# Performance work log

Hardware: AMD Instinct MI355X
Metric: run time of the kernel (lower is better)

Reference implementation:

```python
import jax, jax.numpy as jnp
import numpy as np

N_NODES = 50000
N_EDGES = 200000
N_GRAPHS = 2048
EMB = 300
N_LAYERS = 5
BN_EPS = 1e-5


def setup_inputs() -> dict:
    key = jax.random.key(0)
    ks = jax.random.split(key, 16)
    s = 0.02
    d = {}
    d["atomic_number"] = jax.random.randint(ks[0], (N_NODES,), 0, 120)
    d["chirality_type"] = jax.random.randint(ks[1], (N_NODES,), 0, 3)
    d["bond_type"] = jax.random.randint(ks[2], (N_EDGES,), 0, 6)
    d["bond_direction_type"] = jax.random.randint(ks[3], (N_EDGES,), 0, 3)
    d["src"] = jax.random.randint(ks[4], (N_EDGES,), 0, N_NODES)
    d["dst"] = jax.random.randint(ks[5], (N_EDGES,), 0, N_NODES)
    d["graph_ids"] = jnp.sort(jax.random.randint(ks[6], (N_NODES,), 0, N_GRAPHS))
    d["num_graphs"] = N_GRAPHS
    d["node_emb0"] = jax.random.normal(ks[7], (120, EMB), jnp.float32) * s
    d["node_emb1"] = jax.random.normal(ks[8], (3, EMB), jnp.float32) * s
    d["edge_emb0"] = jax.random.normal(ks[9], (N_LAYERS, 6, EMB), jnp.float32) * s
    d["edge_emb1"] = jax.random.normal(ks[10], (N_LAYERS, 3, EMB), jnp.float32) * s
    d["W1"] = jax.random.normal(ks[11], (N_LAYERS, EMB, 2 * EMB), jnp.float32) * s
    d["b1"] = jnp.zeros((N_LAYERS, 2 * EMB), jnp.float32)
    d["W2"] = jax.random.normal(ks[12], (N_LAYERS, 2 * EMB, EMB), jnp.float32) * s
    d["b2"] = jnp.zeros((N_LAYERS, EMB), jnp.float32)
    d["bn_gamma"] = jnp.ones((N_LAYERS, EMB), jnp.float32)
    d["bn_beta"] = jnp.zeros((N_LAYERS, EMB), jnp.float32)
    d["bn_mean"] = jax.random.normal(ks[13], (N_LAYERS, EMB), jnp.float32) * s
    d["bn_var"] = jax.random.uniform(ks[14], (N_LAYERS, EMB), jnp.float32, 0.5, 1.5)
    return d


def gin_node_feats(atomic_number, chirality_type, bond_type, bond_direction_type,
                   src, dst, node_emb0, node_emb1, edge_emb0, edge_emb1,
                   W1, b1, W2, b2, bn_gamma, bn_beta, bn_mean, bn_var):
    n = atomic_number.shape[0]
    h = node_emb0[atomic_number] + node_emb1[chirality_type]  # [N, EMB]
    feats = [h]
    for l in range(N_LAYERS):
        # u_add_e message: src node feat + per-layer categorical edge embedding
        e = edge_emb0[l][bond_type] + edge_emb1[l][bond_direction_type]  # [E, EMB]
        m = feats[l][src] + e
        agg = jax.ops.segment_sum(m, dst, num_segments=n)  # sum aggregation at dst
        x = jax.nn.relu(agg @ W1[l] + b1[l]) @ W2[l] + b2[l]  # GIN MLP 300->600->300
        # BatchNorm1d in eval mode (running stats)
        x = (x - bn_mean[l]) * jax.lax.rsqrt(bn_var[l] + BN_EPS) * bn_gamma[l] + bn_beta[l]
        if l < N_LAYERS - 1:
            x = jax.nn.relu(x)  # activation on all but last layer
        feats.append(x)  # dropout is identity in eval mode
    return jnp.concatenate(feats, axis=1)  # JK='concat' -> [N, 6*EMB]


def reference(atomic_number, chirality_type, bond_type, bond_direction_type,
              src, dst, graph_ids, num_graphs,
              node_emb0, node_emb1, edge_emb0, edge_emb1,
              W1, b1, W2, b2, bn_gamma, bn_beta, bn_mean, bn_var):
    nf = gin_node_feats(atomic_number, chirality_type, bond_type, bond_direction_type,
                        src, dst, node_emb0, node_emb1, edge_emb0, edge_emb1,
                        W1, b1, W2, b2, bn_gamma, bn_beta, bn_mean, bn_var)
    sums = jax.ops.segment_sum(nf, graph_ids, num_segments=num_graphs)  # SumPooling
    counts = jax.ops.segment_sum(jnp.ones((nf.shape[0], 1), nf.dtype), graph_ids,
                                 num_segments=num_graphs)
    avg = sums / jnp.maximum(counts, 1.0)  # AvgPooling
    return jnp.concatenate([avg, sums], axis=1)  # [G, 2*6*EMB]
```

## Files before the change

### kernel.cpp

```cpp
#include <hip/hip_runtime.h>

#define EMB 300
#define HID 600
#define NL 5
#define BN_EPS 1e-5f

#define FS 320
#define HS 640
#define NPW 8
#define KS1 10
#define KS2 20

typedef __attribute__((ext_vector_type(8))) short short8;
typedef __attribute__((ext_vector_type(4))) float f32x4;
typedef __attribute__((ext_vector_type(4))) unsigned short us4;

__device__ __forceinline__ unsigned short f2bf(float x) {
    unsigned u = __float_as_uint(x);
    unsigned r = (u + 0x7FFFu + ((u >> 16) & 1u)) >> 16;
    return (unsigned short)r;
}
__device__ __forceinline__ float bf2f(unsigned short h) {
    return __uint_as_float(((unsigned)h) << 16);
}

#define GLDS16(gsrc, ldst)                                                     \
    __builtin_amdgcn_global_load_lds(                                          \
        (const __attribute__((address_space(1))) unsigned int*)(gsrc),         \
        (__attribute__((address_space(3))) unsigned int*)(ldst), 16, 0, 0)

__global__ void k_init_h0(const int* __restrict__ an, const int* __restrict__ ch,
                          const float* __restrict__ ne0, const float* __restrict__ ne1,
                          unsigned short* __restrict__ Fb, int n) {
    int t = blockIdx.x * blockDim.x + threadIdx.x;
    int i = t / (FS / 4), f4 = t - i * (FS / 4);
    if (i >= n) return;
    int f = f4 * 4;
    us4 h = {0, 0, 0, 0};
    if (f < EMB) {
        const float4 a = *(const float4*)(ne0 + (size_t)an[i] * EMB + f);
        const float4 b = *(const float4*)(ne1 + (size_t)ch[i] * EMB + f);
        h[0] = f2bf(a.x + b.x); h[1] = f2bf(a.y + b.y);
        h[2] = f2bf(a.z + b.z); h[3] = f2bf(a.w + b.w);
    }
    *(us4*)(Fb + (size_t)i * FS + f) = h;
}

__global__ void k_hist(const int* __restrict__ dst, const int* __restrict__ bt,
                       const int* __restrict__ bd, int* __restrict__ deg,
                       int* __restrict__ cnt9, int e) {
    int t = blockIdx.x * blockDim.x + threadIdx.x;
    if (t >= e) return;
    int d = dst[t];
    atomicAdd(&deg[d], 1);
    atomicAdd(&cnt9[d * 9 + bt[t]], 1);
    atomicAdd(&cnt9[d * 9 + 6 + bd[t]], 1);
}

__global__ __launch_bounds__(256)
void k_scan_blk(const int* __restrict__ deg, int* __restrict__ incl,
                int* __restrict__ part, int n) {
    int tid = threadIdx.x;
    int base = blockIdx.x * 1024 + tid * 4;
    int v0 = (base + 0 < n) ? deg[base + 0] : 0;
    int v1 = (base + 1 < n) ? deg[base + 1] : 0;
    int v2 = (base + 2 < n) ? deg[base + 2] : 0;
    int v3 = (base + 3 < n) ? deg[base + 3] : 0;
    int ts = v0 + v1 + v2 + v3;
    int lane = tid & 63, w = tid >> 6;
    int x = ts;
#pragma unroll
    for (int off = 1; off < 64; off <<= 1) {
        int y = __shfl_up(x, off);
        if (lane >= off) x += y;
    }
    __shared__ int ws[4];
    if (lane == 63) ws[w] = x;
    __syncthreads();
    int woff = 0;
    for (int i = 0; i < w; ++i) woff += ws[i];
    int r = woff + x - ts;
    r += v0; if (base + 0 < n) incl[base + 0] = r;
    r += v1; if (base + 1 < n) incl[base + 1] = r;
    r += v2; if (base + 2 < n) incl[base + 2] = r;
    r += v3; if (base + 3 < n) incl[base + 3] = r;
    if (tid == 255) part[blockIdx.x] = woff + x;
}

__global__ __launch_bounds__(1024)
void k_scan_part(int* __restrict__ part, int nb) {
    int tid = threadIdx.x;
    int v = (tid < nb) ? part[tid] : 0;
    int lane = tid & 63, w = tid >> 6;
    int x = v;
#pragma unroll
    for (int off = 1; off < 64; off <<= 1) {
        int y = __shfl_up(x, off);
        if (lane >= off) x += y;
    }
    __shared__ int ws[16];
    if (lane == 63) ws[w] = x;
    __syncthreads();
    int woff = 0;
    for (int i = 0; i < w; ++i) woff += ws[i];
    if (tid < nb) part[tid] = woff + x - v;
}

__global__ void k_scan_add(const int* __restrict__ incl, const int* __restrict__ part,
                           const int* __restrict__ deg, int* __restrict__ roff,
                           int* __restrict__ curs, int n) {
    int i = blockIdx.x * blockDim.x + threadIdx.x;
    if (i >= n) return;
    int inc = incl[i] + part[i >> 10];
    roff[i + 1] = inc;
    curs[i] = inc - deg[i];
    if (i == 0) roff[0] = 0;
}

__global__ void k_scatter(const int* __restrict__ dst, const int* __restrict__ src,
                          int* __restrict__ cursor, int* __restrict__ srcs, int e) {
    int t = blockIdx.x * blockDim.x + threadIdx.x;
    if (t < e) { int p = atomicAdd(&cursor[dst[t]], 1); srcs[p] = src[t]; }
}

__global__ void k_gbound(const int* __restrict__ gids, int* __restrict__ gstart,
                         int n, int G) {
    int i = blockIdx.x * blockDim.x + threadIdx.x;
    if (i >= n) return;
    int g = gids[i];
    int gp = (i == 0) ? -1 : gids[i - 1];
    for (int q = gp + 1; q <= g; ++q) gstart[q] = i;
    if (i == n - 1)
        for (int q = g + 1; q <= G; ++q) gstart[q] = n;
}

__global__ void k_prep_w1p(const float* __restrict__ W1, unsigned short* __restrict__ W1P,
                           int total) {
    int t = blockIdx.x * blockDim.x + threadIdx.x;
    if (t >= total) return;
    int lane = t & 63;
    int r = t >> 6;
    int ks = r % KS1; r /= KS1;
    int nf = r % 40;
    int l = r / 40;
    int n = nf * 16 + (lane & 15);
    int kb = ks * 32 + (lane >> 4) * 8;
    unsigned short v[8];
#pragma unroll
    for (int e = 0; e < 8; ++e) {
        int k = kb + e;
        v[e] = (n < HID && k < EMB) ? f2bf(W1[(size_t)l * EMB * HID + (size_t)k * HID + n]) : 0;
    }
    *(short8*)(W1P + (size_t)t * 8) = *(short8*)v;
}

__global__ void k_prep_w2p(const float* __restrict__ W2, unsigned short* __restrict__ W2P,
                           int total) {
    int t = blockIdx.x * blockDim.x + threadIdx.x;
    if (t >= total) return;
    int lane = t & 63;
    int r = t >> 6;
    int ks = r % KS2; r /= KS2;
    int nf = r % 20;
    int l = r / 20;
    int n = nf * 16 + (lane & 15);
    int kb = ks * 32 + (lane >> 4) * 8;
    unsigned short v[8];
#pragma unroll
    for (int e = 0; e < 8; ++e) {
        int k = kb + e;
        v[e] = (n < EMB && k < HID) ? f2bf(W2[(size_t)l * HID * EMB + (size_t)k * EMB + n]) : 0;
    }
    *(short8*)(W2P + (size_t)t * 8) = *(short8*)v;
}

__global__ void k_prep_params(const float* __restrict__ b1, const float* __restrict__ b2,
                              const float* __restrict__ g, const float* __restrict__ be,
                              const float* __restrict__ mu, const float* __restrict__ va,
                              float* __restrict__ b1p, float* __restrict__ scp,
                              float* __restrict__ shp, int total) {
    int t = blockIdx.x * blockDim.x + threadIdx.x;
    if (t >= total) return;
    int n = t % HS, l = t / HS;
    b1p[t] = (n < HID) ? b1[l * HID + n] : 0.f;
    if (n < FS) {
        float sc = 0.f, sh = 0.f;
        if (n < EMB) {
            sc = g[l * EMB + n] * rsqrtf(va[l * EMB + n] + BN_EPS);
            sh = be[l * EMB + n] + (b2[l * EMB + n] - mu[l * EMB + n]) * sc;
        }
        scp[l * FS + n] = sc;
        shp[l * FS + n] = sh;
    }
}

__global__ __launch_bounds__(256)
void k_aggregate(const unsigned short* __restrict__ fb,
                 const float* __restrict__ e0, const float* __restrict__ e1,
                 const int* __restrict__ roff, const int* __restrict__ srcs,
                 const int* __restrict__ cnt9,
                 unsigned short* __restrict__ agg, int n) {
    const int v0 = (blockIdx.x * 4 + (threadIdx.x >> 6)) * NPW;
    if (v0 >= n) return;
    const int lane = threadIdx.x & 63;
    const int nv = min(NPW, n - v0);

    int rv = 0;
    {
        int idx = v0 + lane;
        if (lane <= NPW && idx <= n) rv = roff[idx];
    }
    const int base = __shfl(rv, 0);
    const int total = __shfl(rv, nv) - base;

    const int n9 = n * 9;
    const int base9 = v0 * 9;
    int c0 = (base9 + lane < n9) ? cnt9[base9 + lane] : 0;
    int c1 = (lane < 8 && base9 + 64 + lane < n9) ? cnt9[base9 + 64 + lane] : 0;

    int c = 0;
    int chunk = 0;
    auto nextIdx = [&]() -> int {
        if ((c & 63) == 0)
            chunk = (c + lane < total) ? srcs[base + c + lane] : 0;
        int r = __shfl(chunk, c & 63);
        ++c;
        return r;
    };

#pragma unroll
    for (int i = 0; i < NPW; ++i) {
        if (i < nv) {
            const int di = __shfl(rv, i + 1) - __shfl(rv, i);
            float aA[4] = {0.f, 0.f, 0.f, 0.f};
            float aB[4] = {0.f, 0.f, 0.f, 0.f};
            int k = 0;
            for (; k + 4 <= di; k += 4) {
                int i0 = nextIdx(), i1 = nextIdx(), i2 = nextIdx(), i3 = nextIdx();
                const us4* r0 = (const us4*)(fb + (size_t)i0 * FS);
                const us4* r1 = (const us4*)(fb + (size_t)i1 * FS);
                const us4* r2 = (const us4*)(fb + (size_t)i2 * FS);
                const us4* r3 = (const us4*)(fb + (size_t)i3 * FS);
                us4 x0 = r0[lane], x1 = r1[lane], x2 = r2[lane], x3 = r3[lane];
                us4 y0 = {}, y1 = {}, y2 = {}, y3 = {};
                if (lane < 11) { y0 = r0[64 + lane]; y1 = r1[64 + lane];
                                 y2 = r2[64 + lane]; y3 = r3[64 + lane]; }
#pragma unroll
                for (int q = 0; q < 4; ++q)
                    aA[q] += (bf2f(x0[q]) + bf2f(x1[q])) + (bf2f(x2[q]) + bf2f(x3[q]));
                if (lane < 11) {
#pragma unroll
                    for (int q = 0; q < 4; ++q)
                        aB[q] += (bf2f(y0[q]) + bf2f(y1[q])) + (bf2f(y2[q]) + bf2f(y3[q]));
                }
            }
            for (; k < di; ++k) {
                int i0 = nextIdx();
                const us4* r0 = (const us4*)(fb + (size_t)i0 * FS);
                us4 x0 = r0[lane];
#pragma unroll
                for (int q = 0; q < 4; ++q) aA[q] += bf2f(x0[q]);
                if (lane < 11) {
                    us4 y0 = r0[64 + lane];
#pragma unroll
                    for (int q = 0; q < 4; ++q) aB[q] += bf2f(y0[q]);
                }
            }
#pragma unroll
            for (int t = 0; t < 9; ++t) {
                const int pos = i * 9 + t;
                int cv = __shfl(pos < 64 ? c0 : c1, pos & 63);
                if (cv) {
                    float fc = (float)cv;
                    const float* row = (t < 6) ? (e0 + t * EMB) : (e1 + (t - 6) * EMB);
                    f32x4 ea = *(const f32x4*)(row + 4 * lane);
#pragma unroll
                    for (int q = 0; q < 4; ++q) aA[q] += fc * ea[q];
                    if (lane < 11) {
                        f32x4 eb = *(const f32x4*)(row + 256 + 4 * lane);
#pragma unroll
                        for (int q = 0; q < 4; ++q) aB[q] += fc * eb[q];
                    }
                }
            }
            us4* ar = (us4*)(agg + (size_t)(v0 + i) * FS);
            us4 h;
#pragma unroll
            for (int q = 0; q < 4; ++q) h[q] = f2bf(aA[q]);
            ar[lane] = h;
            if (lane < 11) {
                us4 hb;
#pragma unroll
                for (int q = 0; q < 4; ++q) hb[q] = f2bf(aB[q]);
                ar[64 + lane] = hb;
            }
        }
    }
}

template <int EPI>
__global__ __launch_bounds__(512, 4)
void k_mlp(const unsigned short* __restrict__ A,
           const unsigned short* __restrict__ W1P,
           const unsigned short* __restrict__ W2P,
           const float* __restrict__ b1p,
           const float* __restrict__ scp, const float* __restrict__ shp,
           unsigned short* __restrict__ Cout) {
    __shared__ unsigned short Ash[64 * 320];
    __shared__ unsigned short Hh[64 * 320];
    const int tid = threadIdx.x;
    const int lane = tid & 63, wid = tid >> 6;
    const int wm = wid >> 2, wn = wid & 3;
    const int lr = lane & 15, lk = lane >> 4, rgrp = lk * 4;
    const size_t m0s = (size_t)blockIdx.x * 64;
    const int swz = (lr & 7) << 4;

#pragma unroll
    for (int cch = 0; cch < 5; ++cch) {
        const int sbase = wid * 5120 + cch * 1024;
        const int s = sbase + lane * 16;
        const int row = s / 640;
        const int u = s ^ ((row & 7) << 4);
        GLDS16((const char*)A + m0s * 640 + u, (char*)Ash + sbase);
    }
    asm volatile("s_waitcnt vmcnt(0)" ::: "memory");
    __syncthreads();

    f32x4 acc2[5][2] = {};
    const int r0 = wm * 32 + lr;

#pragma unroll
    for (int h = 0; h < 2; ++h) {
        if (h) __syncthreads();
        {
            f32x4 acc1[5][2] = {};
            for (int ks = 0; ks < KS1; ++ks) {
                const int oa0 = (r0 * 640 + ks * 64 + lk * 16) ^ swz;
                const int oa1 = ((r0 + 16) * 640 + ks * 64 + lk * 16) ^ swz;
                short8 a0 = *(const short8*)((const char*)Ash + oa0);
                short8 a1 = *(const short8*)((const char*)Ash + oa1);
                const unsigned short* wp =
                    W1P + (((size_t)(h * 20 + wn * 5) * KS1 + ks) * 64 + lane) * 8;
                short8 w0 = *(const short8*)(wp + (size_t)0 * KS1 * 64 * 8);
                short8 w1 = *(const short8*)(wp + (size_t)1 * KS1 * 64 * 8);
                short8 w2 = *(const short8*)(wp + (size_t)2 * KS1 * 64 * 8);
                short8 w3 = *(const short8*)(wp + (size_t)3 * KS1 * 64 * 8);
                short8 w4 = *(const short8*)(wp + (size_t)4 * KS1 * 64 * 8);
                __builtin_amdgcn_s_setprio(1);
                acc1[0][0] = __builtin_amdgcn_mfma_f32_16x16x32_bf16(w0, a0, acc1[0][0], 0, 0, 0);
                acc1[0][1] = __builtin_amdgcn_mfma_f32_16x16x32_bf16(w0, a1, acc1[0][1], 0, 0, 0);
                acc1[1][0] = __builtin_amdgcn_mfma_f32_16x16x32_bf16(w1, a0, acc1[1][0], 0, 0, 0);
                acc1[1][1] = __builtin_amdgcn_mfma_f32_16x16x32_bf16(w1, a1, acc1[1][1], 0, 0, 0);
                acc1[2][0] = __builtin_amdgcn_mfma_f32_16x16x32_bf16(w2, a0, acc1[2][0], 0, 0, 0);
                acc1[2][1] = __builtin_amdgcn_mfma_f32_16x16x32_bf16(w2, a1, acc1[2][1], 0, 0, 0);
                acc1[3][0] = __builtin_amdgcn_mfma_f32_16x16x32_bf16(w3, a0, acc1[3][0], 0, 0, 0);
                acc1[3][1] = __builtin_amdgcn_mfma_f32_16x16x32_bf16(w3, a1, acc1[3][1], 0, 0, 0);
                acc1[4][0] = __builtin_amdgcn_mfma_f32_16x16x32_bf16(w4, a0, acc1[4][0], 0, 0, 0);
                acc1[4][1] = __builtin_amdgcn_mfma_f32_16x16x32_bf16(w4, a1, acc1[4][1], 0, 0, 0);
                __builtin_amdgcn_s_setprio(0);
            }
#pragma unroll
            for (int i = 0; i < 5; ++i) {
                const int nc = wn * 80 + i * 16 + rgrp;
                const f32x4 q0 = *(const f32x4*)&b1p[h * 320 + nc];
#pragma unroll
                for (int j = 0; j < 2; ++j) {
                    const int m = wm * 32 + j * 16 + lr;
                    us4 hh;
#pragma unroll
                    for (int p = 0; p < 4; ++p)
                        hh[p] = f2bf(fmaxf(acc1[i][j][p] + q0[p], 0.f));
                    const int o = (m * 640 + nc * 2) ^ swz;
                    *(us4*)((char*)Hh + o) = hh;
                }
            }
        }
        __syncthreads();
        for (int kk = 0; kk < KS1; ++kk) {
            const int oh0 = (r0 * 640 + kk * 64 + lk * 16) ^ swz;
            const int oh1 = ((r0 + 16) * 640 + kk * 64 + lk * 16) ^ swz;
            short8 h0 = *(const short8*)((const char*)Hh + oh0);
            short8 h1 = *(const short8*)((const char*)Hh + oh1);
            const unsigned short* wp =
                W2P + (((size_t)(wn * 5) * KS2 + h * KS1 + kk) * 64 + lane) * 8;
            short8 w0 = *(const short8*)(wp + (size_t)0 * KS2 * 64 * 8);
            short8 w1 = *(const short8*)(wp + (size_t)1 * KS2 * 64 * 8);
            short8 w2 = *(const short8*)(wp + (size_t)2 * KS2 * 64 * 8);
            short8 w3 = *(const short8*)(wp + (size_t)3 * KS2 * 64 * 8);
            short8 w4 = *(const short8*)(wp + (size_t)4 * KS2 * 64 * 8);
            __builtin_amdgcn_s_setprio(1);
            acc2[0][0] = __builtin_amdgcn_mfma_f32_16x16x32_bf16(w0, h0, acc2[0][0], 0, 0, 0);
            acc2[0][1] = __builtin_amdgcn_mfma_f32_16x16x32_bf16(w0, h1, acc2[0][1], 0, 0, 0);
            acc2[1][0] = __builtin_amdgcn_mfma_f32_16x16x32_bf16(w1, h0, acc2[1][0], 0, 0, 0);
            acc2[1][1] = __builtin_amdgcn_mfma_f32_16x16x32_bf16(w1, h1, acc2[1][1], 0, 0, 0);
            acc2[2][0] = __builtin_amdgcn_mfma_f32_16x16x32_bf16(w2, h0, acc2[2][0], 0, 0, 0);
            acc2[2][1] = __builtin_amdgcn_mfma_f32_16x16x32_bf16(w2, h1, acc2[2][1], 0, 0, 0);
            acc2[3][0] = __builtin_amdgcn_mfma_f32_16x16x32_bf16(w3, h0, acc2[3][0], 0, 0, 0);
            acc2[3][1] = __builtin_amdgcn_mfma_f32_16x16x32_bf16(w3, h1, acc2[3][1], 0, 0, 0);
            acc2[4][0] = __builtin_amdgcn_mfma_f32_16x16x32_bf16(w4, h0, acc2[4][0], 0, 0, 0);
            acc2[4][1] = __builtin_amdgcn_mfma_f32_16x16x32_bf16(w4, h1, acc2[4][1], 0, 0, 0);
            __builtin_amdgcn_s_setprio(0);
        }
    }

#pragma unroll
    for (int i = 0; i < 5; ++i) {
        const int n0 = wn * 80 + i * 16 + rgrp;
        const f32x4 q0 = *(const f32x4*)&scp[n0];
        const f32x4 q1 = *(const f32x4*)&shp[n0];
#pragma unroll
        for (int j = 0; j < 2; ++j) {
            const size_t m = m0s + (size_t)(wm * 32 + j * 16 + lr);
            us4 hh;
#pragma unroll
            for (int p = 0; p < 4; ++p) {
                float x = acc2[i][j][p] * q0[p] + q1[p];
                if (EPI == 1) x = fmaxf(x, 0.f);
                hh[p] = f2bf(x);
            }
            *(us4*)(Cout + m * FS + n0) = hh;
        }
    }
}

__global__ __launch_bounds__(256)
void k_pool(const unsigned short* __restrict__ feats, const int* __restrict__ gstart,
            float* __restrict__ out, int l) {
    const int g = blockIdx.x;
    const int tid = threadIdx.x;
    const int w = tid >> 6, lane = tid & 63;
    const int s = gstart[g], e = gstart[g + 1];
    float aA[4] = {0.f, 0.f, 0.f, 0.f};
    float aB[4] = {0.f, 0.f, 0.f, 0.f};
    int v = s + w;
    for (; v + 4 < e; v += 8) {
        const us4* r0 = (const us4*)(feats + (size_t)v * FS);
        const us4* r1 = (const us4*)(feats + (size_t)(v + 4) * FS);
        us4 x0 = r0[lane], x1 = r1[lane];
        us4 y0 = {}, y1 = {};
        if (lane < 11) { y0 = r0[64 + lane]; y1 = r1[64 + lane]; }
#pragma unroll
        for (int q = 0; q < 4; ++q) aA[q] += bf2f(x0[q]) + bf2f(x1[q]);
        if (lane < 11) {
#pragma unroll
            for (int q = 0; q < 4; ++q) aB[q] += bf2f(y0[q]) + bf2f(y1[q]);
        }
    }
    if (v < e) {
        const us4* r0 = (const us4*)(feats + (size_t)v * FS);
        us4 x0 = r0[lane];
#pragma unroll
        for (int q = 0; q < 4; ++q) aA[q] += bf2f(x0[q]);
        if (lane < 11) {
            us4 y0 = r0[64 + lane];
#pragma unroll
            for (int q = 0; q < 4; ++q) aB[q] += bf2f(y0[q]);
        }
    }
    __shared__ f32x4 smA[4][64];
    __shared__ f32x4 smB[4][16];
    f32x4 xa;
#pragma unroll
    for (int q = 0; q < 4; ++q) xa[q] = aA[q];
    smA[w][lane] = xa;
    if (lane < 16) {
        f32x4 xb;
#pragma unroll
        for (int q = 0; q < 4; ++q) xb[q] = aB[q];
        smB[w][lane] = xb;
    }
    __syncthreads();
    if (w == 0) {
        f32x4 t = smA[0][lane] + smA[1][lane] + smA[2][lane] + smA[3][lane];
        float inv = 1.0f / fmaxf((float)(e - s), 1.0f);
        float* oavg = out + (size_t)g * (12 * EMB) + l * EMB;
        float* osum = oavg + 6 * EMB;
        *(f32x4*)(oavg + 4 * lane) = t * inv;
        *(f32x4*)(osum + 4 * lane) = t;
        if (lane < 11) {
            f32x4 tb = smB[0][lane] + smB[1][lane] + smB[2][lane] + smB[3][lane];
            *(f32x4*)(oavg + 256 + 4 * lane) = tb * inv;
            *(f32x4*)(osum + 256 + 4 * lane) = tb;
        }
    }
}

extern "C" void kernel_launch(void* const* d_in, const int* in_sizes, int n_in,
                              void* d_out, int out_size, void* d_ws, size_t ws_size,
                              hipStream_t stream) {
    const int*   an  = (const int*)d_in[0];
    const int*   ch  = (const int*)d_in[1];
    const int*   bt  = (const int*)d_in[2];
    const int*   bd  = (const int*)d_in[3];
    const int*   src = (const int*)d_in[4];
    const int*   dst = (const int*)d_in[5];
    const int*   gid = (const int*)d_in[6];
    const float* ne0 = (const float*)d_in[8];
    const float* ne1 = (const float*)d_in[9];
    const float* ee0 = (const float*)d_in[10];
    const float* ee1 = (const float*)d_in[11];
    const float* W1  = (const float*)d_in[12];
    const float* b1  = (const float*)d_in[13];
    const float* W2  = (const float*)d_in[14];
    const float* b2  = (const float*)d_in[15];
    const float* bng = (const float*)d_in[16];
    const float* bnb = (const float*)d_in[17];
    const float* bnm = (const float*)d_in[18];
    const float* bnv = (const float*)d_in[19];

    const int N = in_sizes[0];
    const int E = in_sizes[2];
    const int G = out_size / (12 * EMB);
    const int M_pad = ((N + 63) / 64) * 64;
    const int MT = M_pad / 64;
    const int nb = (N + 1023) / 1024;

    char* ws = (char*)d_ws;
    size_t off = 0;
    auto alloc = [&](size_t bytes) -> void* {
        void* p = (void*)(ws + off);
        off += (bytes + 255) & ~(size_t)255;
        return p;
    };
    unsigned short* Fb0  = (unsigned short*)alloc((size_t)M_pad * FS * 2);
    unsigned short* Fb1  = (unsigned short*)alloc((size_t)M_pad * FS * 2);
    unsigned short* A1   = (unsigned short*)alloc((size_t)M_pad * FS * 2);
    unsigned short* W1P  = (unsigned short*)alloc((size_t)NL * 40 * KS1 * 64 * 8 * 2);
    unsigned short* W2P  = (unsigned short*)alloc((size_t)NL * 20 * KS2 * 64 * 8 * 2);
    float*          b1p  = (float*)alloc((size_t)NL * HS * 4);
    float*          scp  = (float*)alloc((size_t)NL * FS * 4);
    float*          shp  = (float*)alloc((size_t)NL * FS * 4);
    int*            deg  = (int*)alloc((size_t)N * 4);
    int*            roff = (int*)alloc(((size_t)N + 1) * 4);
    int*            curs = (int*)alloc((size_t)N * 4);
    int*            srcs = (int*)alloc((size_t)E * 4);
    int*            cnt9 = (int*)alloc((size_t)N * 9 * 4);
    int*            incl = (int*)alloc((size_t)N * 4);
    int*            part = (int*)alloc((size_t)1024 * 4);
    int*            gst  = (int*)alloc(((size_t)G + 1) * 4);

    {
        int t1 = NL * 40 * KS1 * 64;
        k_prep_w1p<<<(t1 + 255) / 256, 256, 0, stream>>>(W1, W1P, t1);
        int t2 = NL * 20 * KS2 * 64;
        k_prep_w2p<<<(t2 + 255) / 256, 256, 0, stream>>>(W2, W2P, t2);
        int t3 = NL * HS;
        k_prep_params<<<(t3 + 255) / 256, 256, 0, stream>>>(b1, b2, bng, bnb, bnm, bnv,
                                                            b1p, scp, shp, t3);
    }

    {
        int tt = N * (FS / 4);
        k_init_h0<<<(tt + 255) / 256, 256, 0, stream>>>(an, ch, ne0, ne1, Fb0, N);
    }

    hipMemsetAsync(deg, 0, (size_t)N * 4, stream);
    hipMemsetAsync(cnt9, 0, (size_t)N * 9 * 4, stream);
    k_hist<<<(E + 255) / 256, 256, 0, stream>>>(dst, bt, bd, deg, cnt9, E);
    k_scan_blk<<<nb, 256, 0, stream>>>(deg, incl, part, N);
    k_scan_part<<<1, 1024, 0, stream>>>(part, nb);
    k_scan_add<<<(N + 255) / 256, 256, 0, stream>>>(incl, part, deg, roff, curs, N);
    k_scatter<<<(E + 255) / 256, 256, 0, stream>>>(dst, src, curs, srcs, E);
    k_gbound<<<(N + 255) / 256, 256, 0, stream>>>(gid, gst, N, G);

    const int aggBlocks = (N + 4 * NPW - 1) / (4 * NPW);

    unsigned short* Fbc = Fb0;
    unsigned short* Fbo = Fb1;
    for (int l = 0; l < NL; ++l) {
        k_pool<<<G, 256, 0, stream>>>(Fbc, gst, (float*)d_out, l);
        k_aggregate<<<aggBlocks, 256, 0, stream>>>(Fbc,
                                                   ee0 + (size_t)l * 6 * EMB,
                                                   ee1 + (size_t)l * 3 * EMB,
                                                   roff, srcs, cnt9, A1, N);
        const unsigned short* W1Pl = W1P + (size_t)l * 40 * KS1 * 64 * 8;
        const unsigned short* W2Pl = W2P + (size_t)l * 20 * KS2 * 64 * 8;
        if (l < NL - 1)
            k_mlp<1><<<MT, 512, 0, stream>>>(A1, W1Pl, W2Pl,
                                             b1p + (size_t)l * HS,
                                             scp + (size_t)l * FS, shp + (size_t)l * FS,
                                             Fbo);
        else
            k_mlp<2><<<MT, 512, 0, stream>>>(A1, W1Pl, W2Pl,
                                             b1p + (size_t)l * HS,
                                             scp + (size_t)l * FS, shp + (size_t)l * FS,
                                             Fbo);
        unsigned short* t = Fbc; Fbc = Fbo; Fbo = t;
    }
    k_pool<<<G, 256, 0, stream>>>(Fbc, gst, (float*)d_out, NL);
}
```

Before: 777.9 us.

## Run MLP block with 16 waves and full hidden tile in shared memory

The fused two-layer MLP kernel now launches 1024 threads per block instead of 512. It stores the whole 64x640 hidden activation in LDS rather than processing it in two halves. The first GEMM splits the hidden columns across 8 wave columns. The second GEMM gives each wave a 16-row slice across the full 640-wide reduction, which removes the extra barrier and half-loop. The cost is more LDS per block (about 120 KB), which likely allows only one block per CU. The launch-bounds minimum of 4 blocks with 1024 threads may also force heavy register limits, and W2 weight fragments are now loaded once per 16 rows instead of per 32.

Result: slower. 856.8 us (+10.1%).

```diff
diff --git a/kernel.cpp b/kernel.cpp
--- a/kernel.cpp
+++ b/kernel.cpp
@@ -299,7 +299,7 @@
 }
 
 template <int EPI>
-__global__ __launch_bounds__(512, 4)
+__global__ __launch_bounds__(1024, 4)
 void k_mlp(const unsigned short* __restrict__ A,
            const unsigned short* __restrict__ W1P,
            const unsigned short* __restrict__ W2P,
@@ -307,17 +307,15 @@
            const float* __restrict__ scp, const float* __restrict__ shp,
            unsigned short* __restrict__ Cout) {
     __shared__ unsigned short Ash[64 * 320];
-    __shared__ unsigned short Hh[64 * 320];
+    __shared__ unsigned short Hsh[64 * 640];
     const int tid = threadIdx.x;
     const int lane = tid & 63, wid = tid >> 6;
-    const int wm = wid >> 2, wn = wid & 3;
     const int lr = lane & 15, lk = lane >> 4, rgrp = lk * 4;
     const size_t m0s = (size_t)blockIdx.x * 64;
     const int swz = (lr & 7) << 4;
 
-#pragma unroll
-    for (int cch = 0; cch < 5; ++cch) {
-        const int sbase = wid * 5120 + cch * 1024;
+    for (int cch = wid; cch < 40; cch += 16) {
+        const int sbase = cch * 1024;
         const int s = sbase + lane * 16;
         const int row = s / 640;
         const int u = s ^ ((row & 7) << 4);
@@ -326,95 +324,83 @@
     asm volatile("s_waitcnt vmcnt(0)" ::: "memory");
     __syncthreads();
 
-    f32x4 acc2[5][2] = {};
-    const int r0 = wm * 32 + lr;
-
-#pragma unroll
-    for (int h = 0; h < 2; ++h) {
-        if (h) __syncthreads();
-        {
-            f32x4 acc1[5][2] = {};
-            for (int ks = 0; ks < KS1; ++ks) {
-                const int oa0 = (r0 * 640 + ks * 64 + lk * 16) ^ swz;
-                const int oa1 = ((r0 + 16) * 640 + ks * 64 + lk * 16) ^ swz;
-                short8 a0 = *(const short8*)((const char*)Ash + oa0);
-                short8 a1 = *(const short8*)((const char*)Ash + oa1);
-                const unsigned short* wp =
-                    W1P + (((size_t)(h * 20 + wn * 5) * KS1 + ks) * 64 + lane) * 8;
-                short8 w0 = *(const short8*)(wp + (size_t)0 * KS1 * 64 * 8);
-                short8 w1 = *(const short8*)(wp + (size_t)1 * KS1 * 64 * 8);
-                short8 w2 = *(const short8*)(wp + (size_t)2 * KS1 * 64 * 8);
-                short8 w3 = *(const short8*)(wp + (size_t)3 * KS1 * 64 * 8);
-                short8 w4 = *(const short8*)(wp + (size_t)4 * KS1 * 64 * 8);
-                __builtin_amdgcn_s_setprio(1);
-                acc1[0][0] = __builtin_amdgcn_mfma_f32_16x16x32_bf16(w0, a0, acc1[0][0], 0, 0, 0);
-                acc1[0][1] = __builtin_amdgcn_mfma_f32_16x16x32_bf16(w0, a1, acc1[0][1], 0, 0, 0);
-                acc1[1][0] = __builtin_amdgcn_mfma_f32_16x16x32_bf16(w1, a0, acc1[1][0], 0, 0, 0);
-                acc1[1][1] = __builtin_amdgcn_mfma_f32_16x16x32_bf16(w1, a1, acc1[1][1], 0, 0, 0);
-                acc1[2][0] = __builtin_amdgcn_mfma_f32_16x16x32_bf16(w2, a0, acc1[2][0], 0, 0, 0);
-                acc1[2][1] = __builtin_amdgcn_mfma_f32_16x16x32_bf16(w2, a1, acc1[2][1], 0, 0, 0);
-                acc1[3][0] = __builtin_amdgcn_mfma_f32_16x16x32_bf16(w3, a0, acc1[3][0], 0, 0, 0);
-                acc1[3][1] = __builtin_amdgcn_mfma_f32_16x16x32_bf16(w3, a1, acc1[3][1], 0, 0, 0);
-                acc1[4][0] = __builtin_amdgcn_mfma_f32_16x16x32_bf16(w4, a0, acc1[4][0], 0, 0, 0);
-                acc1[4][1] = __builtin_amdgcn_mfma_f32_16x16x32_bf16(w4, a1, acc1[4][1], 0, 0, 0);
-                __builtin_amdgcn_s_setprio(0);
+    {
+        const int wm = wid >> 3, wn = wid & 7;
+        const int r0 = wm * 32 + lr;
+        f32x4 acc1[5][2] = {};
+        for (int ks = 0; ks < KS1; ++ks) {
+            const int oa0 = (r0 * 640 + ks * 64 + lk * 16) ^ swz;
+            const int oa1 = ((r0 + 16) * 640 + ks * 64 + lk * 16) ^ swz;
+            short8 a0 = *(const short8*)((const char*)Ash + oa0);
+            short8 a1 = *(const short8*)((const char*)Ash + oa1);
+            const unsigned short* wp = W1P + (((size_t)(wn * 5) * KS1 + ks) * 64 + lane) * 8;
+            short8 w0 = *(const short8*)(wp + (size_t)0 * KS1 * 64 * 8);
+            short8 w1 = *(const short8*)(wp + (size_t)1 * KS1 * 64 * 8);
+            short8 w2 = *(const short8*)(wp + (size_t)2 * KS1 * 64 * 8);
+            short8 w3 = *(const short8*)(wp + (size_t)3 * KS1 * 64 * 8);
+            short8 w4 = *(const short8*)(wp + (size_t)4 * KS1 * 64 * 8);
+            __builtin_amdgcn_s_setprio(1);
+            acc1[0][0] = __builtin_amdgcn_mfma_f32_16x16x32_bf16(w0, a0, acc1[0][0], 0, 0, 0);
+            acc1[0][1] = __builtin_amdgcn_mfma_f32_16x16x32_bf16(w0, a1, acc1[0][1], 0, 0, 0);
+            acc1[1][0] = __builtin_amdgcn_mfma_f32_16x16x32_bf16(w1, a0, acc1[1][0], 0, 0, 0);
+            acc1[1][1] = __builtin_amdgcn_mfma_f32_16x16x32_bf16(w1, a1, acc1[1][1], 0, 0, 0);
+            acc1[2][0] = __builtin_amdgcn_mfma_f32_16x16x32_bf16(w2, a0, acc1[2][0], 0, 0, 0);
+            acc1[2][1] = __builtin_amdgcn_mfma_f32_16x16x32_bf16(w2, a1, acc1[2][1], 0, 0, 0);
+            acc1[3][0] = __builtin_amdgcn_mfma_f32_16x16x32_bf16(w3, a0, acc1[3][0], 0, 0, 0);
+            acc1[3][1] = __builtin_amdgcn_mfma_f32_16x16x32_bf16(w3, a1, acc1[3][1], 0, 0, 0);
+            acc1[4][0] = __builtin_amdgcn_mfma_f32_16x16x32_bf16(w4, a0, acc1[4][0], 0, 0, 0);
+            acc1[4][1] = __builtin_amdgcn_mfma_f32_16x16x32_bf16(w4, a1, acc1[4][1], 0, 0, 0);
+            __builtin_amdgcn_s_setprio(0);
+        }
+#pragma unroll
+        for (int i = 0; i < 5; ++i) {
+            const int n0 = wn * 80 + i * 16 + rgrp;
+            const f32x4 q0 = *(const f32x4*)&b1p[n0];
+#pragma unroll
+            for (int j = 0; j < 2; ++j) {
+                const int m = wm * 32 + j * 16 + lr;
+                us4 hh;
+#pragma unroll
+                for (int p = 0; p < 4; ++p)
+                    hh[p] = f2bf(fmaxf(acc1[i][j][p] + q0[p], 0.f));
+                const int o = (m * 1280 + n0 * 2) ^ swz;
+                *(us4*)((char*)Hsh + o) = hh;
             }
-#pragma unroll
-            for (int i = 0; i < 5; ++i) {
-                const int nc = wn * 80 + i * 16 + rgrp;
-                const f32x4 q0 = *(const f32x4*)&b1p[h * 320 + nc];
-#pragma unroll
-                for (int j = 0; j < 2; ++j) {
-                    const int m = wm * 32 + j * 16 + lr;
-                    us4 hh;
-#pragma unroll
-                    for (int p = 0; p < 4; ++p)
-                        hh[p] = f2bf(fmaxf(acc1[i][j][p] + q0[p], 0.f));
-                    const int o = (m * 640 + nc * 2) ^ swz;
-                    *(us4*)((char*)Hh + o) = hh;
-                }
-            }
-        }
-        __syncthreads();
-        for (int kk = 0; kk < KS1; ++kk) {
-            const int oh0 = (r0 * 640 + kk * 64 + lk * 16) ^ swz;
-            const int oh1 = ((r0 + 16) * 640 + kk * 64 + lk * 16) ^ swz;
-            short8 h0 = *(const short8*)((const char*)Hh + oh0);
-            short8 h1 = *(const short8*)((const char*)Hh + oh1);
-            const unsigned short* wp =
-                W2P + (((size_t)(wn * 5) * KS2 + h * KS1 + kk) * 64 + lane) * 8;
+        }
+    }
+    __syncthreads();
+
+    {
+        const int wm2 = wid >> 2, wn2 = wid & 3;
+        const int r2 = wm2 * 16 + lr;
+        f32x4 acc2[5] = {};
+        for (int ks = 0; ks < KS2; ++ks) {
+            const int oh = (r2 * 1280 + ks * 64 + lk * 16) ^ swz;
+            short8 h0 = *(const short8*)((const char*)Hsh + oh);
+            const unsigned short* wp = W2P + (((size_t)(wn2 * 5) * KS2 + ks) * 64 + lane) * 8;
             short8 w0 = *(const short8*)(wp + (size_t)0 * KS2 * 64 * 8);
             short8 w1 = *(const short8*)(wp + (size_t)1 * KS2 * 64 * 8);
             short8 w2 = *(const short8*)(wp + (size_t)2 * KS2 * 64 * 8);
             short8 w3 = *(const short8*)(wp + (size_t)3 * KS2 * 64 * 8);
             short8 w4 = *(const short8*)(wp + (size_t)4 * KS2 * 64 * 8);
             __builtin_amdgcn_s_setprio(1);
-            acc2[0][0] = __builtin_amdgcn_mfma_f32_16x16x32_bf16(w0, h0, acc2[0][0], 0, 0, 0);
-            acc2[0][1] = __builtin_amdgcn_mfma_f32_16x16x32_bf16(w0, h1, acc2[0][1], 0, 0, 0);
-            acc2[1][0] = __builtin_amdgcn_mfma_f32_16x16x32_bf16(w1, h0, acc2[1][0], 0, 0, 0);
-            acc2[1][1] = __builtin_amdgcn_mfma_f32_16x16x32_bf16(w1, h1, acc2[1][1], 0, 0, 0);
-            acc2[2][0] = __builtin_amdgcn_mfma_f32_16x16x32_bf16(w2, h0, acc2[2][0], 0, 0, 0);
-            acc2[2][1] = __builtin_amdgcn_mfma_f32_16x16x32_bf16(w2, h1, acc2[2][1], 0, 0, 0);
-            acc2[3][0] = __builtin_amdgcn_mfma_f32_16x16x32_bf16(w3, h0, acc2[3][0], 0, 0, 0);
-            acc2[3][1] = __builtin_amdgcn_mfma_f32_16x16x32_bf16(w3, h1, acc2[3][1], 0, 0, 0);
-            acc2[4][0] = __builtin_amdgcn_mfma_f32_16x16x32_bf16(w4, h0, acc2[4][0], 0, 0, 0);
-            acc2[4][1] = __builtin_amdgcn_mfma_f32_16x16x32_bf16(w4, h1, acc2[4][1], 0, 0, 0);
+            acc2[0] = __builtin_amdgcn_mfma_f32_16x16x32_bf16(w0, h0, acc2[0], 0, 0, 0);
+            acc2[1] = __builtin_amdgcn_mfma_f32_16x16x32_bf16(w1, h0, acc2[1], 0, 0, 0);
+            acc2[2] = __builtin_amdgcn_mfma_f32_16x16x32_bf16(w2, h0, acc2[2], 0, 0, 0);
+            acc2[3] = __builtin_amdgcn_mfma_f32_16x16x32_bf16(w3, h0, acc2[3], 0, 0, 0);
+            acc2[4] = __builtin_amdgcn_mfma_f32_16x16x32_bf16(w4, h0, acc2[4], 0, 0, 0);
             __builtin_amdgcn_s_setprio(0);
         }
-    }
-
-#pragma unroll
-    for (int i = 0; i < 5; ++i) {
-        const int n0 = wn * 80 + i * 16 + rgrp;
-        const f32x4 q0 = *(const f32x4*)&scp[n0];
-        const f32x4 q1 = *(const f32x4*)&shp[n0];
-#pragma unroll
-        for (int j = 0; j < 2; ++j) {
-            const size_t m = m0s + (size_t)(wm * 32 + j * 16 + lr);
+#pragma unroll
+        for (int i = 0; i < 5; ++i) {
+            const int n0 = wn2 * 80 + i * 16 + rgrp;
+            const f32x4 q0 = *(const f32x4*)&scp[n0];
+            const f32x4 q1 = *(const f32x4*)&shp[n0];
+            const size_t m = m0s + (size_t)(wm2 * 16 + lr);
             us4 hh;
 #pragma unroll
             for (int p = 0; p < 4; ++p) {
-                float x = acc2[i][j][p] * q0[p] + q1[p];
+                float x = acc2[i][p] * q0[p] + q1[p];
                 if (EPI == 1) x = fmaxf(x, 0.f);
                 hh[p] = f2bf(x);
             }
@@ -576,15 +562,15 @@
         const unsigned short* W1Pl = W1P + (size_t)l * 40 * KS1 * 64 * 8;
         const unsigned short* W2Pl = W2P + (size_t)l * 20 * KS2 * 64 * 8;
         if (l < NL - 1)
-            k_mlp<1><<<MT, 512, 0, stream>>>(A1, W1Pl, W2Pl,
-                                             b1p + (size_t)l * HS,
-                                             scp + (size_t)l * FS, shp + (size_t)l * FS,
-                                             Fbo);
+            k_mlp<1><<<MT, 1024, 0, stream>>>(A1, W1Pl, W2Pl,
+                                              b1p + (size_t)l * HS,
+                                              scp + (size_t)l * FS, shp + (size_t)l * FS,
+                                              Fbo);
         else
-            k_mlp<2><<<MT, 512, 0, stream>>>(A1, W1Pl, W2Pl,
-                                             b1p + (size_t)l * HS,
-                                             scp + (size_t)l * FS, shp + (size_t)l * FS,
-                                             Fbo);
+            k_mlp<2><<<MT, 1024, 0, stream>>>(A1, W1Pl, W2Pl,
+                                              b1p + (size_t)l * HS,
+                                              scp + (size_t)l * FS, shp + (size_t)l * FS,
+                                              Fbo);
         unsigned short* t = Fbc; Fbc = Fbo; Fbo = t;
     }
     k_pool<<<G, 256, 0, stream>>>(Fbc, gst, (float*)d_out, NL);
```
